# Performance work log

Hardware: AMD Instinct MI355X
Metric: run time of the kernel (lower is better)

Reference implementation:

```python
import jax, jax.numpy as jnp
import numpy as np

NEG_SLOPE = 0.2  # LeakyReLU slope

def setup_inputs() -> dict:
    key = jax.random.key(0)
    k1, k2, k3, k4, k5 = jax.random.split(key, 5)
    H, hidden, code_dim, n_codes = 4, 256, 512, 200000
    return {
        "provider_emb": jax.random.normal(k1, (1, code_dim), dtype=jnp.float32),
        "code_embs": jax.random.normal(k2, (n_codes, code_dim), dtype=jnp.float32),
        "Ws": jax.random.normal(k3, (H, hidden, code_dim), dtype=jnp.float32) * 0.05,
        "bs": jax.random.normal(k4, (H, hidden), dtype=jnp.float32) * 0.05,
        "a_s": jax.random.normal(k5, (H, 2 * hidden), dtype=jnp.float32),
    }

def reference(provider_emb, code_embs, Ws, bs, a_s):
    # Ws: [H, hidden, code_dim], bs: [H, hidden], a_s: [H, 2*hidden]
    hidden = Ws.shape[1]
    a1 = a_s[:, :hidden]   # applied to provider part  [H, hidden]
    a2 = a_s[:, hidden:]   # applied to code part      [H, hidden]
    # provider_h: [H, hidden]
    provider_h = jnp.einsum('hdc,c->hd', Ws, provider_emb[0]) + bs
    # code_h: [H, n, hidden]
    code_h = jnp.einsum('hdc,nc->hnd', Ws, code_embs) + bs[:, None, :]
    # e_i = leaky_relu(provider_h . a1 + code_h_i . a2)  -> [H, n]
    p_score = jnp.einsum('hd,hd->h', provider_h, a1)            # [H]
    c_score = jnp.einsum('hnd,hd->hn', code_h, a2)              # [H, n]
    e = p_score[:, None] + c_score
    e = jnp.where(e >= 0, e, NEG_SLOPE * e)                     # leaky_relu(0.2)
    alpha = jax.nn.softmax(e, axis=1)                           # softmax over codes (dim 0 in torch)
    return alpha  # [num_heads, n_codes]
```

## Files before the change

kernel.cpp:

```cpp
#include <hip/hip_runtime.h>
#include <hip/hip_bf16.h>

#define H     4
#define HID   256
#define CDIM  512
#define NCH   16
#define DPER  (HID / NCH)
#define NB    2048

#define WS_P1   0
#define WS_P2   (WS_P1 + H * NCH * CDIM)
#define WS_W2   (WS_P2 + H * NCH * CDIM)
#define WS_PRE  (WS_W2 + H * CDIM)
#define WS_GMAX (WS_PRE + H)
#define WS_GINV (WS_GMAX + H)
#define WS_BMS  (WS_GINV + H)

__global__ void __launch_bounds__(256) prepA_kernel(
    const float* __restrict__ Ws, const float* __restrict__ as_,
    float* __restrict__ ws)
{
    int h = blockIdx.x >> 4, chunk = blockIdx.x & (NCH - 1);
    int t = threadIdx.x;
    const float* W  = Ws + ((size_t)h * HID + chunk * DPER) * CDIM;
    const float* a1 = as_ + (size_t)h * 2 * HID + chunk * DPER;
    const float* a2 = a1 + HID;
    int c0 = t, c1 = t + 256;
    float w1a = 0.f, w1b = 0.f, w2a = 0.f, w2b = 0.f;
#pragma unroll
    for (int d = 0; d < DPER; ++d) {
        float x0 = W[d * CDIM + c0], x1 = W[d * CDIM + c1];
        float v1 = a1[d], v2 = a2[d];
        w1a = fmaf(v1, x0, w1a); w2a = fmaf(v2, x0, w2a);
        w1b = fmaf(v1, x1, w1b); w2b = fmaf(v2, x1, w2b);
    }
    size_t base = (size_t)(h * NCH + chunk) * CDIM;
    ws[WS_P1 + base + c0] = w1a; ws[WS_P1 + base + c1] = w1b;
    ws[WS_P2 + base + c0] = w2a; ws[WS_P2 + base + c1] = w2b;
}

__global__ void __launch_bounds__(256) prepB_kernel(
    const float* __restrict__ pe, const float* __restrict__ bs,
    const float* __restrict__ as_, float* __restrict__ ws)
{
    int h = blockIdx.x;
    int t = threadIdx.x;
    int c0 = t, c1 = t + 256;
    float w1a = 0.f, w1b = 0.f, w2a = 0.f, w2b = 0.f;
#pragma unroll
    for (int k = 0; k < NCH; ++k) {
        size_t base = (size_t)(h * NCH + k) * CDIM;
        w1a += ws[WS_P1 + base + c0]; w1b += ws[WS_P1 + base + c1];
        w2a += ws[WS_P2 + base + c0]; w2b += ws[WS_P2 + base + c1];
    }
    ws[WS_W2 + h * CDIM + c0] = w2a;
    ws[WS_W2 + h * CDIM + c1] = w2b;
    const float* a1 = as_ + (size_t)h * 2 * HID;
    const float* a2 = a1 + HID;
    float contrib = w1a * pe[c0] + w1b * pe[c1];
    contrib += bs[h * HID + t] * (a1[t] + a2[t]);
    __shared__ float red[256];
    red[t] = contrib;
    __syncthreads();
    for (int s2 = 128; s2 > 0; s2 >>= 1) {
        if (t < s2) red[t] += red[t + s2];
        __syncthreads();
    }
    if (t == 0) ws[WS_PRE + h] = red[0];
}

__global__ void __launch_bounds__(256) score_kernel(
    const float* __restrict__ codes, const float* __restrict__ ws_in,
    float* __restrict__ e_out, float* __restrict__ ws_out, int n_codes)
{
    const int lane = threadIdx.x & 63;
    const int wid  = threadIdx.x >> 6;
    const int gw   = blockIdx.x * 4 + wid;
    const int Wtot = gridDim.x * 4;

    float4 w2a[H], w2b[H];
#pragma unroll
    for (int h = 0; h < H; ++h) {
        w2a[h] = *(const float4*)&ws_in[WS_W2 + h * CDIM + 4 * lane];
        w2b[h] = *(const float4*)&ws_in[WS_W2 + h * CDIM + 256 + 4 * lane];
    }
    const bool b0 = lane & 1, b1 = lane & 2;
    float mypre;
    {
        float p0 = ws_in[WS_PRE + 0], p1 = ws_in[WS_PRE + 1];
        float p2 = ws_in[WS_PRE + 2], p3 = ws_in[WS_PRE + 3];
        float t01 = b0 ? p1 : p0, t23 = b0 ? p3 : p2;
        mypre = b1 ? t23 : t01;
    }

    float m = -1e30f, s = 0.f;
    const int npairs = n_codes >> 1;

    for (int p = gw; p < npairs; p += Wtot) {
        const int n0 = 2 * p;
        const float4* r0 = (const float4*)(codes + (size_t)n0 * CDIM);
        const float4* r1 = (const float4*)(codes + (size_t)(n0 + 1) * CDIM);
        float4 xa0 = r0[lane], xb0 = r0[64 + lane];
        float4 xa1 = r1[lane], xb1 = r1[64 + lane];

        float A0[H], A1[H];
#pragma unroll
        for (int h = 0; h < H; ++h) {
            A0[h] = xa0.x * w2a[h].x + xa0.y * w2a[h].y +
                    xa0.z * w2a[h].z + xa0.w * w2a[h].w +
                    xb0.x * w2b[h].x + xb0.y * w2b[h].y +
                    xb0.z * w2b[h].z + xb0.w * w2b[h].w;
            A1[h] = xa1.x * w2a[h].x + xa1.y * w2a[h].y +
                    xa1.z * w2a[h].z + xa1.w * w2a[h].w +
                    xb1.x * w2b[h].x + xb1.y * w2b[h].y +
                    xb1.z * w2b[h].z + xb1.w * w2b[h].w;
        }
#pragma unroll
        for (int h = 0; h < H; ++h) {
            A0[h] += __shfl_xor(A0[h], 1, 64);
            A0[h] += __shfl_xor(A0[h], 2, 64);
            A1[h] += __shfl_xor(A1[h], 1, 64);
            A1[h] += __shfl_xor(A1[h], 2, 64);
        }
        float t01 = b0 ? A0[1] : A0[0], t23 = b0 ? A0[3] : A0[2];
        float v0 = b1 ? t23 : t01;
        t01 = b0 ? A1[1] : A1[0]; t23 = b0 ? A1[3] : A1[2];
        float v1 = b1 ? t23 : t01;
#pragma unroll
        for (int msk = 4; msk <= 32; msk <<= 1) {
            v0 += __shfl_xor(v0, msk, 64);
            v1 += __shfl_xor(v1, msk, 64);
        }
        float e0 = mypre + v0; e0 = e0 >= 0.f ? e0 : 0.2f * e0;
        float e1 = mypre + v1; e1 = e1 >= 0.f ? e1 : 0.2f * e1;
        float mm = fmaxf(m, fmaxf(e0, e1));
        s = s * __expf(m - mm) + __expf(e0 - mm) + __expf(e1 - mm);
        m = mm;
        if (lane < H) {
            float2 ev = make_float2(e0, e1);
            *(float2*)&e_out[(size_t)lane * n_codes + n0] = ev;
        }
    }
    if ((n_codes & 1) && gw == 0) {
        const int n0 = n_codes - 1;
        const float4* r0 = (const float4*)(codes + (size_t)n0 * CDIM);
        float4 xa0 = r0[lane], xb0 = r0[64 + lane];
        float A0[H];
#pragma unroll
        for (int h = 0; h < H; ++h) {
            A0[h] = xa0.x * w2a[h].x + xa0.y * w2a[h].y +
                    xa0.z * w2a[h].z + xa0.w * w2a[h].w +
                    xb0.x * w2b[h].x + xb0.y * w2b[h].y +
                    xb0.z * w2b[h].z + xb0.w * w2b[h].w;
            A0[h] += __shfl_xor(A0[h], 1, 64);
            A0[h] += __shfl_xor(A0[h], 2, 64);
        }
        float t01 = b0 ? A0[1] : A0[0], t23 = b0 ? A0[3] : A0[2];
        float v0 = b1 ? t23 : t01;
#pragma unroll
        for (int msk = 4; msk <= 32; msk <<= 1) v0 += __shfl_xor(v0, msk, 64);
        float e0 = mypre + v0; e0 = e0 >= 0.f ? e0 : 0.2f * e0;
        float mm = fmaxf(m, e0);
        s = s * __expf(m - mm) + __expf(e0 - mm);
        m = mm;
        if (lane < H) e_out[(size_t)lane * n_codes + n0] = e0;
    }

    __shared__ float lm[4][H], ls[4][H];
    if (lane < H) { lm[wid][lane] = m; ls[wid][lane] = s; }
    __syncthreads();
    if (threadIdx.x < H) {
        int h = threadIdx.x;
        float M = -1e30f, S = 0.f;
#pragma unroll
        for (int w = 0; w < 4; ++w) {
            float mm = fmaxf(M, lm[w][h]);
            S = S * __expf(M - mm) + ls[w][h] * __expf(lm[w][h] - mm);
            M = mm;
        }
        float2 v = make_float2(M, S);
        *(float2*)&ws_out[WS_BMS + (size_t)(h * NB + blockIdx.x) * 2] = v;
    }
}

__global__ void __launch_bounds__(256) sreduce_kernel(float* __restrict__ ws)
{
    int lane = threadIdx.x & 63;
    int h    = threadIdx.x >> 6;
    float M = -1e30f, S = 0.f;
    for (int i = lane; i < NB; i += 64) {
        float2 v = *(const float2*)&ws[WS_BMS + (size_t)(h * NB + i) * 2];
        float mm = fmaxf(M, v.x);
        S = S * __expf(M - mm) + v.y * __expf(v.x - mm);
        M = mm;
    }
    for (int msk = 32; msk; msk >>= 1) {
        float M2 = __shfl_xor(M, msk, 64);
        float S2 = __shfl_xor(S, msk, 64);
        float mm = fmaxf(M, M2);
        S = S * __expf(M - mm) + S2 * __expf(M2 - mm);
        M = mm;
    }
    if (lane == 0) { ws[WS_GMAX + h] = M; ws[WS_GINV + h] = 1.f / S; }
}

__global__ void __launch_bounds__(256) norm_kernel(
    float* __restrict__ e, const float* __restrict__ ws, int n_codes)
{
    int i = blockIdx.x * blockDim.x + threadIdx.x;
    int perh = n_codes >> 2;
    int tot = H * perh;
    if (i >= tot) return;
    int h = i / perh;
    float gm = ws[WS_GMAX + h], gi = ws[WS_GINV + h];
    float4 v = ((float4*)e)[i];
    v.x = __expf(v.x - gm) * gi;
    v.y = __expf(v.y - gm) * gi;
    v.z = __expf(v.z - gm) * gi;
    v.w = __expf(v.w - gm) * gi;
    ((float4*)e)[i] = v;
}

extern "C" void kernel_launch(void* const* d_in, const int* in_sizes, int n_in,
                              void* d_out, int out_size, void* d_ws, size_t ws_size,
                              hipStream_t stream)
{
    const float* pe    = (const float*)d_in[0];
    const float* codes = (const float*)d_in[1];
    const float* Ws    = (const float*)d_in[2];
    const float* bs    = (const float*)d_in[3];
    const float* as_   = (const float*)d_in[4];
    float* out = (float*)d_out;
    float* ws  = (float*)d_ws;
    int n_codes = in_sizes[1] / CDIM;

    prepA_kernel<<<H * NCH, 256, 0, stream>>>(Ws, as_, ws);
    prepB_kernel<<<H, 256, 0, stream>>>(pe, bs, as_, ws);
    score_kernel<<<NB, 256, 0, stream>>>(codes, ws, out, ws, n_codes);
    sreduce_kernel<<<1, 256, 0, stream>>>(ws);
    int tot4 = (H * n_codes) / 4;
    norm_kernel<<<(tot4 + 255) / 256, 256, 0, stream>>>(out, ws, n_codes);
}
```

Baseline: 102.0 us.

## Use contiguous per-wave code ranges, nontemporal loads, and a merged shuffle reduction

Each wave now processes a contiguous range of code pairs instead of a grid-strided one, and reads code rows with nontemporal vector loads to avoid polluting the cache with streamed data. The cross-lane reduction merges the two codes of a pair into one value after the xor-4 step, cutting shuffles and per-code softmax work; each lane group now tracks its own running max/sum, and these are merged at the end with an extra shuffle. The prep kernel also splits the hidden dimension into twice as many chunks for more parallelism. The odd-tail handling was moved to the last wave and adjusted to the new lane mapping.

```diff
diff --git a/kernel.cpp b/kernel.cpp
--- a/kernel.cpp
+++ b/kernel.cpp
@@ -4,9 +4,11 @@
 #define H     4
 #define HID   256
 #define CDIM  512
-#define NCH   16
+#define NCH   32
 #define DPER  (HID / NCH)
 #define NB    2048
+
+typedef float f32x4 __attribute__((ext_vector_type(4)));
 
 #define WS_P1   0
 #define WS_P2   (WS_P1 + H * NCH * CDIM)
@@ -20,7 +22,7 @@
     const float* __restrict__ Ws, const float* __restrict__ as_,
     float* __restrict__ ws)
 {
-    int h = blockIdx.x >> 4, chunk = blockIdx.x & (NCH - 1);
+    int h = blockIdx.x >> 5, chunk = blockIdx.x & (NCH - 1);
     int t = threadIdx.x;
     const float* W  = Ws + ((size_t)h * HID + chunk * DPER) * CDIM;
     const float* a1 = as_ + (size_t)h * 2 * HID + chunk * DPER;
@@ -76,32 +78,30 @@
     const int lane = threadIdx.x & 63;
     const int wid  = threadIdx.x >> 6;
     const int gw   = blockIdx.x * 4 + wid;
-    const int Wtot = gridDim.x * 4;
-
-    float4 w2a[H], w2b[H];
+    const long long Wtot = (long long)gridDim.x * 4;
+
+    f32x4 w2a[H], w2b[H];
 #pragma unroll
     for (int h = 0; h < H; ++h) {
-        w2a[h] = *(const float4*)&ws_in[WS_W2 + h * CDIM + 4 * lane];
-        w2b[h] = *(const float4*)&ws_in[WS_W2 + h * CDIM + 256 + 4 * lane];
-    }
-    const bool b0 = lane & 1, b1 = lane & 2;
-    float mypre;
-    {
-        float p0 = ws_in[WS_PRE + 0], p1 = ws_in[WS_PRE + 1];
-        float p2 = ws_in[WS_PRE + 2], p3 = ws_in[WS_PRE + 3];
-        float t01 = b0 ? p1 : p0, t23 = b0 ? p3 : p2;
-        mypre = b1 ? t23 : t01;
-    }
+        w2a[h] = *(const f32x4*)&ws_in[WS_W2 + h * CDIM + 4 * lane];
+        w2b[h] = *(const f32x4*)&ws_in[WS_W2 + h * CDIM + 256 + 4 * lane];
+    }
+    const int  hsel = lane & 3;
+    const bool b0 = lane & 1, b1 = lane & 2, b2 = lane & 4;
+    const float mypre = ws_in[WS_PRE + hsel];
+
+    const long long npairs = (long long)n_codes >> 1;
+    const long long ps = (long long)gw * npairs / Wtot;
+    const long long pe_ = ((long long)gw + 1) * npairs / Wtot;
 
     float m = -1e30f, s = 0.f;
-    const int npairs = n_codes >> 1;
-
-    for (int p = gw; p < npairs; p += Wtot) {
-        const int n0 = 2 * p;
-        const float4* r0 = (const float4*)(codes + (size_t)n0 * CDIM);
-        const float4* r1 = (const float4*)(codes + (size_t)(n0 + 1) * CDIM);
-        float4 xa0 = r0[lane], xb0 = r0[64 + lane];
-        float4 xa1 = r1[lane], xb1 = r1[64 + lane];
+
+    for (long long p = ps; p < pe_; ++p) {
+        const f32x4* r = (const f32x4*)(codes + ((size_t)p << 1) * CDIM);
+        f32x4 xa0 = __builtin_nontemporal_load(&r[lane]);
+        f32x4 xb0 = __builtin_nontemporal_load(&r[64 + lane]);
+        f32x4 xa1 = __builtin_nontemporal_load(&r[128 + lane]);
+        f32x4 xb1 = __builtin_nontemporal_load(&r[192 + lane]);
 
         float A0[H], A1[H];
 #pragma unroll
@@ -123,47 +123,61 @@
             A1[h] += __shfl_xor(A1[h], 2, 64);
         }
         float t01 = b0 ? A0[1] : A0[0], t23 = b0 ? A0[3] : A0[2];
-        float v0 = b1 ? t23 : t01;
+        float B0 = b1 ? t23 : t01;
         t01 = b0 ? A1[1] : A1[0]; t23 = b0 ? A1[3] : A1[2];
-        float v1 = b1 ? t23 : t01;
-#pragma unroll
-        for (int msk = 4; msk <= 32; msk <<= 1) {
-            v0 += __shfl_xor(v0, msk, 64);
-            v1 += __shfl_xor(v1, msk, 64);
-        }
-        float e0 = mypre + v0; e0 = e0 >= 0.f ? e0 : 0.2f * e0;
-        float e1 = mypre + v1; e1 = e1 >= 0.f ? e1 : 0.2f * e1;
-        float mm = fmaxf(m, fmaxf(e0, e1));
-        s = s * __expf(m - mm) + __expf(e0 - mm) + __expf(e1 - mm);
+        float B1 = b1 ? t23 : t01;
+        B0 += __shfl_xor(B0, 4, 64);
+        B1 += __shfl_xor(B1, 4, 64);
+        float C = b2 ? B1 : B0;
+        C += __shfl_xor(C, 8, 64);
+        C += __shfl_xor(C, 16, 64);
+        C += __shfl_xor(C, 32, 64);
+
+        float e = mypre + C;
+        e = e >= 0.f ? e : 0.2f * e;
+        float mm = fmaxf(m, e);
+        s = s * __expf(m - mm) + __expf(e - mm);
         m = mm;
-        if (lane < H) {
-            float2 ev = make_float2(e0, e1);
-            *(float2*)&e_out[(size_t)lane * n_codes + n0] = ev;
-        }
-    }
-    if ((n_codes & 1) && gw == 0) {
+        if (!(lane & 56)) {
+            e_out[(size_t)hsel * n_codes + ((size_t)p << 1) + (b2 ? 1 : 0)] = e;
+        }
+    }
+
+    if ((n_codes & 1) && gw == Wtot - 1) {
         const int n0 = n_codes - 1;
-        const float4* r0 = (const float4*)(codes + (size_t)n0 * CDIM);
-        float4 xa0 = r0[lane], xb0 = r0[64 + lane];
-        float A0[H];
+        const f32x4* r = (const f32x4*)(codes + (size_t)n0 * CDIM);
+        f32x4 xa = __builtin_nontemporal_load(&r[lane]);
+        f32x4 xb = __builtin_nontemporal_load(&r[64 + lane]);
+        float A[H];
 #pragma unroll
         for (int h = 0; h < H; ++h) {
-            A0[h] = xa0.x * w2a[h].x + xa0.y * w2a[h].y +
-                    xa0.z * w2a[h].z + xa0.w * w2a[h].w +
-                    xb0.x * w2b[h].x + xb0.y * w2b[h].y +
-                    xb0.z * w2b[h].z + xb0.w * w2b[h].w;
-            A0[h] += __shfl_xor(A0[h], 1, 64);
-            A0[h] += __shfl_xor(A0[h], 2, 64);
-        }
-        float t01 = b0 ? A0[1] : A0[0], t23 = b0 ? A0[3] : A0[2];
-        float v0 = b1 ? t23 : t01;
-#pragma unroll
-        for (int msk = 4; msk <= 32; msk <<= 1) v0 += __shfl_xor(v0, msk, 64);
-        float e0 = mypre + v0; e0 = e0 >= 0.f ? e0 : 0.2f * e0;
-        float mm = fmaxf(m, e0);
-        s = s * __expf(m - mm) + __expf(e0 - mm);
+            A[h] = xa.x * w2a[h].x + xa.y * w2a[h].y +
+                   xa.z * w2a[h].z + xa.w * w2a[h].w +
+                   xb.x * w2b[h].x + xb.y * w2b[h].y +
+                   xb.z * w2b[h].z + xb.w * w2b[h].w;
+            A[h] += __shfl_xor(A[h], 1, 64);
+            A[h] += __shfl_xor(A[h], 2, 64);
+        }
+        float t01 = b0 ? A[1] : A[0], t23 = b0 ? A[3] : A[2];
+        float v = b1 ? t23 : t01;
+#pragma unroll
+        for (int msk = 4; msk <= 32; msk <<= 1) v += __shfl_xor(v, msk, 64);
+        float e = mypre + v;
+        e = e >= 0.f ? e : 0.2f * e;
+        if (!b2) {
+            float mm = fmaxf(m, e);
+            s = s * __expf(m - mm) + __expf(e - mm);
+            m = mm;
+        }
+        if (lane < H) e_out[(size_t)hsel * n_codes + n0] = e;
+    }
+
+    {
+        float M2 = __shfl_xor(m, 4, 64);
+        float S2 = __shfl_xor(s, 4, 64);
+        float mm = fmaxf(m, M2);
+        s = s * __expf(m - mm) + S2 * __expf(M2 - mm);
         m = mm;
-        if (lane < H) e_out[(size_t)lane * n_codes + n0] = e0;
     }
 
     __shared__ float lm[4][H], ls[4][H];
```

Result: faster. 98.41 us (-3.5%).
